# Optimization experiments

Measured on AMD Instinct MI355X. Metric: run time of the kernel, lower is better.

## Reference

```python
import jax, jax.numpy as jnp
import numpy as np

E = 16          # num_local_experts
K = 4           # experts_per_token
H = 2048        # hidden_size
I = 2048        # intermediate_size
LIMIT = 7.0     # swiglu_limit
ALPHA = 1.702   # glu_alpha


def setup_inputs() -> dict:
    key = jax.random.key(0)
    ks = jax.random.split(key, 9)
    int8 = lambda k, shp: jax.random.randint(k, shp, -127, 128).astype(jnp.float32)
    return {
        "hidden_states": jax.random.normal(ks[0], (1024, H), dtype=jnp.float32),
        "router_logits": jax.random.normal(ks[1], (1024, E), dtype=jnp.float32),
        "gate_up_proj": int8(ks[2], (E, H, 2 * I)),                      # int8 values in f32
        "gate_up_proj_scale": jax.random.uniform(ks[3], (E, 2 * I), minval=0.5, maxval=1.5) * 0.002,
        "gate_up_proj_bias": jax.random.normal(ks[4], (E, 2 * I), dtype=jnp.float32) * 0.01,
        "gate_up_smooth_scale": jnp.ones((E, I), dtype=jnp.float32),
        "down_proj": int8(ks[5], (E, I, H)),
        "down_proj_scale": jax.random.uniform(ks[6], (E, H), minval=0.5, maxval=1.5) * 0.002,
        "down_proj_bias": jax.random.normal(ks[7], (E, H), dtype=jnp.float32) * 0.01,
    }


def _dyn_quant(x):
    # per-token symmetric int8 dynamic quant (npu_dynamic_quant)
    scale = jnp.maximum(jnp.max(jnp.abs(x), axis=-1, keepdims=True) / 127.0, 1e-8)
    q = jnp.clip(jnp.round(x / scale), -127.0, 127.0)
    return q, scale


def reference(hidden_states, router_logits, gate_up_proj, gate_up_proj_scale,
              gate_up_proj_bias, gate_up_smooth_scale, down_proj,
              down_proj_scale, down_proj_bias):
    T = hidden_states.shape[0]
    C = (2 * T * K) // E

    # --- gating (npu_moe_gating_top_k: softmax + top-k, then renormalize) ---
    probs = jax.nn.softmax(router_logits, axis=-1)
    topk_w, topk_i = jax.lax.top_k(probs, K)                 # [T,K]
    topk_w = topk_w / jnp.sum(topk_w, axis=-1, keepdims=True)

    # --- per-token dynamic quant ---
    x_q, x_scale = _dyn_quant(hidden_states)                 # [T,H], [T,1]

    # --- dispatch (npu_moe_init_routing_v2): token-major expansion, capacity buckets ---
    flat_e = topk_i.reshape(-1)                              # [T*K] expert id per row
    flat_w = topk_w.reshape(-1)                              # [T*K]
    src = jnp.arange(T * K) // K                             # [T*K] source token
    onehot = jax.nn.one_hot(flat_e, E, dtype=jnp.int32)      # [T*K,E]
    pos = jnp.sum(jnp.cumsum(onehot, axis=0) * onehot, axis=1) - 1  # position within expert
    valid = pos < C
    slot = flat_e * C + jnp.where(valid, pos, 0)             # unique for valid rows
    vf = valid.astype(x_q.dtype)[:, None]
    x_disp = jnp.zeros((E * C, H), x_q.dtype).at[slot].add(x_q[src] * vf)
    s_disp = jnp.zeros((E * C, 1), x_scale.dtype).at[slot].add(x_scale[src] * vf)
    x_disp = x_disp.reshape(E, C, H)
    s_disp = s_disp.reshape(E, C, 1)

    gu_i32 = jnp.einsum('ech,ehf->ecf', x_disp, gate_up_proj)          # [E,C,2I]
    y = gu_i32 * s_disp * gate_up_proj_scale[:, None, :] + gate_up_proj_bias[:, None, :]

    # --- gpt-oss swiglu (activate_left, clamp_limit, alpha=1.702, glu_bias=1.0) ---
    gate = jnp.minimum(y[..., :I], LIMIT)
    up = jnp.clip(y[..., I:], -LIMIT, LIMIT)
    act = gate * jax.nn.sigmoid(ALPHA * gate) * (up + 1.0)
    act = act * gate_up_smooth_scale[:, None, :]

    # --- requant + grouped GEMM 2 + dequant ---
    h_q, h_scale = _dyn_quant(act)                                     # [E,C,I], [E,C,1]
    z_i32 = jnp.einsum('eci,eih->ech', h_q, down_proj)                 # [E,C,H]
    z = z_i32 * h_scale * down_proj_scale[:, None, :] + down_proj_bias[:, None, :]

    # --- combine (npu_moe_finalize_routing): weighted scatter-add per source token ---
    gathered = z.reshape(E * C, H)[slot]                               # [T*K,H]
    out = jnp.zeros((T, H), z.dtype).at[src].add(flat_w[:, None] * vf * gathered)
    return out
```

## Files before the change

### kernel.cpp

```cpp
#include <hip/hip_runtime.h>
#include <stdint.h>
#include <stddef.h>

#define T_TOK 1024
#define NE    16
#define TOPK  4
#define HID   2048
#define INTER 2048
#define CAP   512
#define GLIMIT 7.0f
#define GALPHA 1.702f

#define BM  128
#define BK  64

typedef __attribute__((ext_vector_type(4))) int   iv4;

typedef const __attribute__((address_space(1))) unsigned gl_u32;
typedef __attribute__((address_space(3))) unsigned lds_u32;
__device__ __forceinline__ void gl_lds16(const void* g, void* l) {
    __builtin_amdgcn_global_load_lds((gl_u32*)g, (lds_u32*)l, 16, 0, 0);
}

__device__ __forceinline__ int pack4(float a, float b, float c, float d) {
    int qa = (int)a, qb = (int)b, qc = (int)c, qd = (int)d;
    return (qa & 255) | ((qb & 255) << 8) | ((qc & 255) << 16) | (qd << 24);
}

__global__ __launch_bounds__(256) void gating_kernel(
    const float* __restrict__ logits, int* __restrict__ topki, float* __restrict__ topkw)
{
    int t = blockIdx.x * 256 + threadIdx.x;
    if (t >= T_TOK) return;
    float l[NE];
#pragma unroll
    for (int e = 0; e < NE; e++) l[e] = logits[t * NE + e];
    unsigned used = 0;
    float val[TOPK]; int idx[TOPK];
#pragma unroll
    for (int k = 0; k < TOPK; k++) {
        float bv = -3.4e38f; int bi = 0;
#pragma unroll
        for (int e = 0; e < NE; e++) {
            bool ok = (((used >> e) & 1u) == 0u) && (l[e] > bv);
            bv = ok ? l[e] : bv;
            bi = ok ? e : bi;
        }
        used |= (1u << bi); idx[k] = bi; val[k] = bv;
    }
    float m = val[0];
    float s = 0.f, w[TOPK];
#pragma unroll
    for (int k = 0; k < TOPK; k++) { w[k] = expf(val[k] - m); s += w[k]; }
    float inv = 1.0f / s;
#pragma unroll
    for (int k = 0; k < TOPK; k++) { topki[t * TOPK + k] = idx[k]; topkw[t * TOPK + k] = w[k] * inv; }
}

__global__ __launch_bounds__(256) void quant_x_kernel(
    const float* __restrict__ x, char* __restrict__ xq, float* __restrict__ xs)
{
    int t = blockIdx.x;
    const float4* row = (const float4*)(x + (size_t)t * HID);
    __shared__ float red[256];
    float4 v0 = row[threadIdx.x];
    float4 v1 = row[threadIdx.x + 256];
    float amax = fmaxf(fmaxf(fabsf(v0.x), fabsf(v0.y)), fmaxf(fabsf(v0.z), fabsf(v0.w)));
    amax = fmaxf(amax, fmaxf(fmaxf(fabsf(v1.x), fabsf(v1.y)), fmaxf(fabsf(v1.z), fabsf(v1.w))));
    red[threadIdx.x] = amax; __syncthreads();
    for (int s = 128; s > 0; s >>= 1) {
        if (threadIdx.x < s) red[threadIdx.x] = fmaxf(red[threadIdx.x], red[threadIdx.x + s]);
        __syncthreads();
    }
    float scale = fmaxf(red[0] / 127.0f, 1e-8f);
    if (threadIdx.x == 0) xs[t] = scale;
    char4* orow = (char4*)(xq + (size_t)t * HID);
    {
        char4 c;
        c.x = (char)fminf(fmaxf(rintf(v0.x / scale), -127.f), 127.f);
        c.y = (char)fminf(fmaxf(rintf(v0.y / scale), -127.f), 127.f);
        c.z = (char)fminf(fmaxf(rintf(v0.z / scale), -127.f), 127.f);
        c.w = (char)fminf(fmaxf(rintf(v0.w / scale), -127.f), 127.f);
        orow[threadIdx.x] = c;
        c.x = (char)fminf(fmaxf(rintf(v1.x / scale), -127.f), 127.f);
        c.y = (char)fminf(fmaxf(rintf(v1.y / scale), -127.f), 127.f);
        c.z = (char)fminf(fmaxf(rintf(v1.z / scale), -127.f), 127.f);
        c.w = (char)fminf(fmaxf(rintf(v1.w / scale), -127.f), 127.f);
        orow[threadIdx.x + 256] = c;
    }
}

__global__ __launch_bounds__(1024) void routing_kernel(
    const int* __restrict__ topki, const float* __restrict__ topkw,
    int* __restrict__ row_src, float* __restrict__ row_w, int* __restrict__ counts)
{
    int wv = threadIdx.x >> 6;
    int lane = threadIdx.x & 63;
    int base = 0;
    for (int r0 = 0; r0 < T_TOK * TOPK; r0 += 64) {
        int r = r0 + lane;
        int e = topki[r];
        unsigned long long mask = __ballot(e == wv);
        int pre = __popcll(mask & ((1ULL << lane) - 1ULL));
        if (e == wv) {
            int pos = base + pre;
            if (pos < CAP) {
                row_src[wv * CAP + pos] = r >> 2;
                row_w[wv * CAP + pos] = topkw[r];
            }
        }
        base += __popcll(mask);
    }
    if (lane == 0) counts[wv] = (base < CAP) ? base : CAP;
}

__global__ __launch_bounds__(256) void gemm1_kernel(
    const char* __restrict__ xq, const float* __restrict__ xs,
    const int* __restrict__ row_src, const int* __restrict__ counts,
    const float* __restrict__ gup, const float* __restrict__ gus,
    const float* __restrict__ gub, const float* __restrict__ smo,
    float* __restrict__ act)
{
    int nt = blockIdx.x;
    int mt = blockIdx.y;
    int e  = blockIdx.z;
    int count = counts[e];
    int m0 = mt * BM;
    if (m0 >= count) return;

    __shared__ char sA[BM * BK];
    __shared__ char sB[128 * BK];

    int t = threadIdx.x;
    int lane = t & 63, w = t >> 6;
    int n16 = lane & 15, quad = lane >> 4;
    int swq = quad ^ ((n16 >> 1) & 3);

    const char* aSrc[2];
#pragma unroll
    for (int op = 0; op < 2; op++) {
        int c = op * 256 + t;
        int row = c >> 2, ks = c & 3;
        int ksg = ks ^ ((row >> 1) & 3);
        int gr = m0 + row;
        if (gr > count - 1) gr = count - 1;
        aSrc[op] = xq + (size_t)row_src[e * CAP + gr] * HID + ksg * 16;
    }

    int bn = t >> 1;
    int kb = (t & 1) * 32;
    int colg = nt * 64 + (bn & 63) + ((bn >= 64) ? INTER : 0);
    const float* bsrc = gup + (size_t)e * HID * (2 * INTER) + colg;
    int sn = (bn >> 1) & 3;
    char* wp0 = sB + bn * 64 + (((kb >> 4) + 0) ^ sn) * 16;
    char* wp1 = sB + bn * 64 + (((kb >> 4) + 1) ^ sn) * 16;

    iv4 acc[2][8];
#pragma unroll
    for (int i = 0; i < 2; i++)
#pragma unroll
        for (int j = 0; j < 8; j++) acc[i][j] = (iv4)0;

    for (int k0 = 0; k0 < HID; k0 += BK) {
        float f[32];
#pragma unroll
        for (int i = 0; i < 32; i++)
            f[i] = bsrc[(size_t)(k0 + kb + i) * (2 * INTER)];
        __syncthreads();
        gl_lds16(aSrc[0] + k0, sA + w * 1024);
        gl_lds16(aSrc[1] + k0, sA + 4096 + w * 1024);
        int d[8];
#pragma unroll
        for (int j = 0; j < 8; j++)
            d[j] = pack4(f[4 * j], f[4 * j + 1], f[4 * j + 2], f[4 * j + 3]);
        *(int4*)wp0 = make_int4(d[0], d[1], d[2], d[3]);
        *(int4*)wp1 = make_int4(d[4], d[5], d[6], d[7]);
        __syncthreads();

        iv4 af[2], bf[8];
#pragma unroll
        for (int mf = 0; mf < 2; mf++)
            af[mf] = *(const iv4*)(sA + (w * 32 + mf * 16 + n16) * 64 + swq * 16);
#pragma unroll
        for (int nf = 0; nf < 8; nf++)
            bf[nf] = *(const iv4*)(sB + (nf * 16 + n16) * 64 + swq * 16);
#pragma unroll
        for (int mf = 0; mf < 2; mf++)
#pragma unroll
            for (int nf = 0; nf < 8; nf++)
                acc[mf][nf] = __builtin_amdgcn_mfma_i32_16x16x64_i8(af[mf], bf[nf], acc[mf][nf], 0, 0, 0);
    }

    const float* gsc = gus + (size_t)e * (2 * INTER);
    const float* gbi = gub + (size_t)e * (2 * INTER);
    const float* sms = smo + (size_t)e * INTER;
#pragma unroll
    for (int mf = 0; mf < 2; mf++) {
#pragma unroll
        for (int r = 0; r < 4; r++) {
            int gr = m0 + w * 32 + mf * 16 + quad * 4 + r;
            if (gr >= count) continue;
            float srow = xs[row_src[e * CAP + gr]];
            float* arow = act + (size_t)(e * CAP + gr) * INTER;
#pragma unroll
            for (int g = 0; g < 4; g++) {
                int col = nt * 64 + g * 16 + n16;
                float yg = (float)acc[mf][g][r]     * srow * gsc[col]         + gbi[col];
                float yu = (float)acc[mf][g + 4][r] * srow * gsc[INTER + col] + gbi[INTER + col];
                float gate = fminf(yg, GLIMIT);
                float up   = fminf(fmaxf(yu, -GLIMIT), GLIMIT);
                float sig  = 1.0f / (1.0f + expf(-GALPHA * gate));
                arow[col] = gate * sig * (up + 1.0f) * sms[col];
            }
        }
    }
}

__global__ __launch_bounds__(256) void requant_kernel(
    const float* __restrict__ act, const int* __restrict__ counts,
    char* __restrict__ hq, float* __restrict__ hs)
{
    int b = blockIdx.x;
    int e = b >> 9, c = b & (CAP - 1);
    if (c >= counts[e]) return;
    const float4* row = (const float4*)(act + (size_t)b * INTER);
    __shared__ float red[256];
    float4 v0 = row[threadIdx.x];
    float4 v1 = row[threadIdx.x + 256];
    float amax = fmaxf(fmaxf(fabsf(v0.x), fabsf(v0.y)), fmaxf(fabsf(v0.z), fabsf(v0.w)));
    amax = fmaxf(amax, fmaxf(fmaxf(fabsf(v1.x), fabsf(v1.y)), fmaxf(fabsf(v1.z), fabsf(v1.w))));
    red[threadIdx.x] = amax; __syncthreads();
    for (int s = 128; s > 0; s >>= 1) {
        if (threadIdx.x < s) red[threadIdx.x] = fmaxf(red[threadIdx.x], red[threadIdx.x + s]);
        __syncthreads();
    }
    float scale = fmaxf(red[0] / 127.0f, 1e-8f);
    if (threadIdx.x == 0) hs[b] = scale;
    char4* orow = (char4*)(hq + (size_t)b * INTER);
    {
        char4 cc;
        cc.x = (char)fminf(fmaxf(rintf(v0.x / scale), -127.f), 127.f);
        cc.y = (char)fminf(fmaxf(rintf(v0.y / scale), -127.f), 127.f);
        cc.z = (char)fminf(fmaxf(rintf(v0.z / scale), -127.f), 127.f);
        cc.w = (char)fminf(fmaxf(rintf(v0.w / scale), -127.f), 127.f);
        orow[threadIdx.x] = cc;
        cc.x = (char)fminf(fmaxf(rintf(v1.x / scale), -127.f), 127.f);
        cc.y = (char)fminf(fmaxf(rintf(v1.y / scale), -127.f), 127.f);
        cc.z = (char)fminf(fmaxf(rintf(v1.z / scale), -127.f), 127.f);
        cc.w = (char)fminf(fmaxf(rintf(v1.w / scale), -127.f), 127.f);
        orow[threadIdx.x + 256] = cc;
    }
}

__global__ __launch_bounds__(256) void gemm2_kernel(
    const char* __restrict__ hq, const float* __restrict__ hs,
    const int* __restrict__ row_src, const float* __restrict__ row_w,
    const int* __restrict__ counts, const float* __restrict__ dwn,
    const float* __restrict__ dsc, const float* __restrict__ dbi,
    float* __restrict__ out)
{
    int nt = blockIdx.x;
    int mt = blockIdx.y;
    int e  = blockIdx.z;
    int count = counts[e];
    int m0 = mt * BM;
    if (m0 >= count) return;

    __shared__ char sA[BM * BK];
    __shared__ char sB[128 * BK];

    int t = threadIdx.x;
    int lane = t & 63, w = t >> 6;
    int n16 = lane & 15, quad = lane >> 4;
    int swq = quad ^ ((n16 >> 1) & 3);

    const char* aSrc[2];
#pragma unroll
    for (int op = 0; op < 2; op++) {
        int c = op * 256 + t;
        int row = c >> 2, ks = c & 3;
        int ksg = ks ^ ((row >> 1) & 3);
        int gr = m0 + row;
        if (gr > count - 1) gr = count - 1;
        aSrc[op] = hq + (size_t)(e * CAP + gr) * INTER + ksg * 16;
    }

    int bn = t >> 1;
    int kb = (t & 1) * 32;
    int colg = nt * 128 + bn;
    const float* bsrc = dwn + (size_t)e * INTER * HID + colg;
    int sn = (bn >> 1) & 3;
    char* wp0 = sB + bn * 64 + (((kb >> 4) + 0) ^ sn) * 16;
    char* wp1 = sB + bn * 64 + (((kb >> 4) + 1) ^ sn) * 16;

    iv4 acc[2][8];
#pragma unroll
    for (int i = 0; i < 2; i++)
#pragma unroll
        for (int j = 0; j < 8; j++) acc[i][j] = (iv4)0;

    for (int k0 = 0; k0 < INTER; k0 += BK) {
        float f[32];
#pragma unroll
        for (int i = 0; i < 32; i++)
            f[i] = bsrc[(size_t)(k0 + kb + i) * HID];
        __syncthreads();
        gl_lds16(aSrc[0] + k0, sA + w * 1024);
        gl_lds16(aSrc[1] + k0, sA + 4096 + w * 1024);
        int d[8];
#pragma unroll
        for (int j = 0; j < 8; j++)
            d[j] = pack4(f[4 * j], f[4 * j + 1], f[4 * j + 2], f[4 * j + 3]);
        *(int4*)wp0 = make_int4(d[0], d[1], d[2], d[3]);
        *(int4*)wp1 = make_int4(d[4], d[5], d[6], d[7]);
        __syncthreads();

        iv4 af[2], bf[8];
#pragma unroll
        for (int mf = 0; mf < 2; mf++)
            af[mf] = *(const iv4*)(sA + (w * 32 + mf * 16 + n16) * 64 + swq * 16);
#pragma unroll
        for (int nf = 0; nf < 8; nf++)
            bf[nf] = *(const iv4*)(sB + (nf * 16 + n16) * 64 + swq * 16);
#pragma unroll
        for (int mf = 0; mf < 2; mf++)
#pragma unroll
            for (int nf = 0; nf < 8; nf++)
                acc[mf][nf] = __builtin_amdgcn_mfma_i32_16x16x64_i8(af[mf], bf[nf], acc[mf][nf], 0, 0, 0);
    }

    const float* dscE = dsc + (size_t)e * HID;
    const float* dbiE = dbi + (size_t)e * HID;
#pragma unroll
    for (int mf = 0; mf < 2; mf++) {
#pragma unroll
        for (int r = 0; r < 4; r++) {
            int gr = m0 + w * 32 + mf * 16 + quad * 4 + r;
            if (gr >= count) continue;
            int ri = e * CAP + gr;
            float hsr = hs[ri];
            float wr  = row_w[ri];
            float* orow = out + (size_t)row_src[ri] * HID;
#pragma unroll
            for (int nf = 0; nf < 8; nf++) {
                int col = nt * 128 + nf * 16 + n16;
                float z = (float)acc[mf][nf][r] * hsr * dscE[col] + dbiE[col];
                atomicAdd(&orow[col], wr * z);
            }
        }
    }
}

extern "C" void kernel_launch(void* const* d_in, const int* in_sizes, int n_in,
                              void* d_out, int out_size, void* d_ws, size_t ws_size,
                              hipStream_t stream)
{
    (void)in_sizes; (void)n_in; (void)out_size; (void)ws_size;
    const float* x   = (const float*)d_in[0];
    const float* rl  = (const float*)d_in[1];
    const float* gup = (const float*)d_in[2];
    const float* gus = (const float*)d_in[3];
    const float* gub = (const float*)d_in[4];
    const float* smo = (const float*)d_in[5];
    const float* dwn = (const float*)d_in[6];
    const float* dsc = (const float*)d_in[7];
    const float* dbi = (const float*)d_in[8];
    float* out = (float*)d_out;

    char* p = (char*)d_ws;
    auto carve = [&](size_t bytes) -> char* {
        char* r = p; p += (bytes + 255) & ~(size_t)255; return r;
    };
    char* xq       = carve((size_t)T_TOK * HID);
    float* xs      = (float*)carve((size_t)T_TOK * 4);
    int* topki     = (int*)carve((size_t)T_TOK * TOPK * 4);
    float* topkw   = (float*)carve((size_t)T_TOK * TOPK * 4);
    int* counts    = (int*)carve((size_t)NE * 4);
    int* rsrc      = (int*)carve((size_t)NE * CAP * 4);
    float* rw      = (float*)carve((size_t)NE * CAP * 4);
    float* actb    = (float*)carve((size_t)NE * CAP * INTER * 4);
    char* hq       = carve((size_t)NE * CAP * INTER);
    float* hsb     = (float*)carve((size_t)NE * CAP * 4);

    hipMemsetAsync(d_out, 0, (size_t)T_TOK * HID * 4, stream);
    gating_kernel<<<dim3((T_TOK + 255) / 256), 256, 0, stream>>>(rl, topki, topkw);
    quant_x_kernel<<<dim3(T_TOK), 256, 0, stream>>>(x, xq, xs);
    routing_kernel<<<dim3(1), 1024, 0, stream>>>(topki, topkw, rsrc, rw, counts);
    gemm1_kernel<<<dim3(INTER / 64, CAP / BM, NE), 256, 0, stream>>>(
        xq, xs, rsrc, counts, gup, gus, gub, smo, actb);
    requant_kernel<<<dim3(NE * CAP), 256, 0, stream>>>(actb, counts, hq, hsb);
    gemm2_kernel<<<dim3(HID / 128, CAP / BM, NE), 256, 0, stream>>>(
        hq, hsb, rsrc, rw, counts, dwn, dsc, dbi, out);
}
```

Before: 1.180 ms.

## Prefetch next B tile into registers and remap loads for coalescing

Both grouped GEMM kernels now load the next k-tile of f32 weights into registers while the MFMAs for the current tile run, instead of loading and then stalling before each tile. The thread-to-column mapping also changes so consecutive lanes read consecutive columns of a row, which gives coalesced global loads where the old layout had each thread striding down a column. The prefetch keeps 32 floats live across the MFMA loop, which adds register pressure and may lower occupancy.

Result: faster. 1.066 ms (-9.7%).

```diff
diff --git a/kernel.cpp b/kernel.cpp
--- a/kernel.cpp
+++ b/kernel.cpp
@@ -147,13 +147,12 @@
         aSrc[op] = xq + (size_t)row_src[e * CAP + gr] * HID + ksg * 16;
     }
 
-    int bn = t >> 1;
-    int kb = (t & 1) * 32;
-    int colg = nt * 64 + (bn & 63) + ((bn >= 64) ? INTER : 0);
-    const float* bsrc = gup + (size_t)e * HID * (2 * INTER) + colg;
-    int sn = (bn >> 1) & 3;
-    char* wp0 = sB + bn * 64 + (((kb >> 4) + 0) ^ sn) * 16;
-    char* wp1 = sB + bn * 64 + (((kb >> 4) + 1) ^ sn) * 16;
+    int bc = t & 63;
+    const float* bgate = gup + (size_t)e * HID * (2 * INTER) + nt * 64 + bc;
+    const float* bup   = bgate + INTER;
+    int sn = (bc >> 1) & 3;
+    char* wpg = sB + bc * 64        + (w ^ sn) * 16;
+    char* wpu = sB + (64 + bc) * 64 + (w ^ sn) * 16;
 
     iv4 acc[2][8];
 #pragma unroll
@@ -161,20 +160,27 @@
 #pragma unroll
         for (int j = 0; j < 8; j++) acc[i][j] = (iv4)0;
 
-    for (int k0 = 0; k0 < HID; k0 += BK) {
-        float f[32];
-#pragma unroll
-        for (int i = 0; i < 32; i++)
-            f[i] = bsrc[(size_t)(k0 + kb + i) * (2 * INTER)];
-        __syncthreads();
-        gl_lds16(aSrc[0] + k0, sA + w * 1024);
-        gl_lds16(aSrc[1] + k0, sA + 4096 + w * 1024);
-        int d[8];
-#pragma unroll
-        for (int j = 0; j < 8; j++)
-            d[j] = pack4(f[4 * j], f[4 * j + 1], f[4 * j + 2], f[4 * j + 3]);
-        *(int4*)wp0 = make_int4(d[0], d[1], d[2], d[3]);
-        *(int4*)wp1 = make_int4(d[4], d[5], d[6], d[7]);
+    float f[32];
+#pragma unroll
+    for (int i = 0; i < 16; i++) {
+        f[i]      = bgate[(size_t)(w * 16 + i) * (2 * INTER)];
+        f[16 + i] = bup  [(size_t)(w * 16 + i) * (2 * INTER)];
+    }
+
+    for (int kt = 0; kt < HID / BK; kt++) {
+        __syncthreads();
+        gl_lds16(aSrc[0] + kt * BK, sA + w * 1024);
+        gl_lds16(aSrc[1] + kt * BK, sA + 4096 + w * 1024);
+        {
+            int d0[4], d1[4];
+#pragma unroll
+            for (int j = 0; j < 4; j++) {
+                d0[j] = pack4(f[4 * j],      f[4 * j + 1],      f[4 * j + 2],      f[4 * j + 3]);
+                d1[j] = pack4(f[16 + 4 * j], f[16 + 4 * j + 1], f[16 + 4 * j + 2], f[16 + 4 * j + 3]);
+            }
+            *(int4*)wpg = make_int4(d0[0], d0[1], d0[2], d0[3]);
+            *(int4*)wpu = make_int4(d1[0], d1[1], d1[2], d1[3]);
+        }
         __syncthreads();
 
         iv4 af[2], bf[8];
@@ -184,6 +190,15 @@
 #pragma unroll
         for (int nf = 0; nf < 8; nf++)
             bf[nf] = *(const iv4*)(sB + (nf * 16 + n16) * 64 + swq * 16);
+
+        int kn = (kt + 1 < HID / BK) ? (kt + 1) : kt;
+        size_t krow = (size_t)(kn * BK) * (2 * INTER);
+#pragma unroll
+        for (int i = 0; i < 16; i++) {
+            f[i]      = bgate[krow + (size_t)(w * 16 + i) * (2 * INTER)];
+            f[16 + i] = bup  [krow + (size_t)(w * 16 + i) * (2 * INTER)];
+        }
+
 #pragma unroll
         for (int mf = 0; mf < 2; mf++)
 #pragma unroll
@@ -285,13 +300,12 @@
         aSrc[op] = hq + (size_t)(e * CAP + gr) * INTER + ksg * 16;
     }
 
-    int bn = t >> 1;
-    int kb = (t & 1) * 32;
-    int colg = nt * 128 + bn;
-    const float* bsrc = dwn + (size_t)e * INTER * HID + colg;
-    int sn = (bn >> 1) & 3;
-    char* wp0 = sB + bn * 64 + (((kb >> 4) + 0) ^ sn) * 16;
-    char* wp1 = sB + bn * 64 + (((kb >> 4) + 1) ^ sn) * 16;
+    int bc = t & 127;
+    int half = t >> 7;
+    const float* bsrc = dwn + (size_t)e * INTER * HID + nt * 128 + bc;
+    int sn = (bc >> 1) & 3;
+    char* wp0 = sB + bc * 64 + ((half * 2 + 0) ^ sn) * 16;
+    char* wp1 = sB + bc * 64 + ((half * 2 + 1) ^ sn) * 16;
 
     iv4 acc[2][8];
 #pragma unroll
@@ -299,20 +313,23 @@
 #pragma unroll
         for (int j = 0; j < 8; j++) acc[i][j] = (iv4)0;
 
-    for (int k0 = 0; k0 < INTER; k0 += BK) {
-        float f[32];
-#pragma unroll
-        for (int i = 0; i < 32; i++)
-            f[i] = bsrc[(size_t)(k0 + kb + i) * HID];
-        __syncthreads();
-        gl_lds16(aSrc[0] + k0, sA + w * 1024);
-        gl_lds16(aSrc[1] + k0, sA + 4096 + w * 1024);
-        int d[8];
-#pragma unroll
-        for (int j = 0; j < 8; j++)
-            d[j] = pack4(f[4 * j], f[4 * j + 1], f[4 * j + 2], f[4 * j + 3]);
-        *(int4*)wp0 = make_int4(d[0], d[1], d[2], d[3]);
-        *(int4*)wp1 = make_int4(d[4], d[5], d[6], d[7]);
+    float f[32];
+#pragma unroll
+    for (int i = 0; i < 32; i++)
+        f[i] = bsrc[(size_t)(half * 32 + i) * HID];
+
+    for (int kt = 0; kt < INTER / BK; kt++) {
+        __syncthreads();
+        gl_lds16(aSrc[0] + kt * BK, sA + w * 1024);
+        gl_lds16(aSrc[1] + kt * BK, sA + 4096 + w * 1024);
+        {
+            int d[8];
+#pragma unroll
+            for (int j = 0; j < 8; j++)
+                d[j] = pack4(f[4 * j], f[4 * j + 1], f[4 * j + 2], f[4 * j + 3]);
+            *(int4*)wp0 = make_int4(d[0], d[1], d[2], d[3]);
+            *(int4*)wp1 = make_int4(d[4], d[5], d[6], d[7]);
+        }
         __syncthreads();
 
         iv4 af[2], bf[8];
@@ -322,6 +339,13 @@
 #pragma unroll
         for (int nf = 0; nf < 8; nf++)
             bf[nf] = *(const iv4*)(sB + (nf * 16 + n16) * 64 + swq * 16);
+
+        int kn = (kt + 1 < INTER / BK) ? (kt + 1) : kt;
+        size_t krow = (size_t)(kn * BK) * HID;
+#pragma unroll
+        for (int i = 0; i < 32; i++)
+            f[i] = bsrc[krow + (size_t)(half * 32 + i) * HID];
+
 #pragma unroll
         for (int mf = 0; mf < 2; mf++)
 #pragma unroll
```
